# Kernel tuning notes

Hardware: AMD Instinct MI355X
Metric: run time of the kernel (lower is better)

Reference implementation:

```python
import jax, jax.numpy as jnp
import numpy as np
import math

WS = 7          # window size (hardcoded in RelativeSinusoidalEmbeddings)
NUM_HEADS = 12

def _rel_embeddings(ws=WS):
    # Faithful replica of RelativeSinusoidalEmbeddings.__init__
    C = 2 * ws - 1
    B = np.zeros((C, C), dtype=np.float32)
    positions = np.arange(C, dtype=np.float32)[:, None]
    divisor = np.exp(np.arange(0, C, 2, dtype=np.float32) * (-math.log(10000.0) / C))
    angles = positions * divisor
    B[:, 0::2] = np.sin(angles)
    B[:, 1::2] = np.cos(angles[:, :-1])
    x = np.arange(1.0, ws + 1.0, 1.0 / ws)                 # length ws*ws
    xi = (x[None, :] - x[:, None]).astype(np.int32)        # trunc toward zero, like torch .int()
    y = np.concatenate([np.arange(1, ws + 1)] * ws)
    yi = y[None, :] - y[:, None]
    return jnp.asarray(B[xi, yi])                           # [ws^2, ws^2]

def _shift_masks(ws=WS):
    n = ws * ws
    s = ws * (ws // 2)
    row = np.zeros((n, n), dtype=np.float32)
    row[-s:, : n - s] = -np.inf
    row[: n - s, -s:] = -np.inf
    # rearrange '(r w1) (c w2) -> (w1 r) (w2 c)'
    col = row.reshape(ws, ws, ws, ws).transpose(1, 0, 3, 2).reshape(n, n)
    return jnp.asarray(row), jnp.asarray(col)

_EMB = _rel_embeddings()
_ROW_MASK, _COL_MASK = _shift_masks()

def setup_inputs() -> dict:
    key = jax.random.key(0)
    k1, k2, k3 = jax.random.split(key, 3)
    B, H, W, D = 16, 56, 56, 384
    return {
        "x": jax.random.normal(k1, (B, H, W, D), dtype=jnp.float32),
        "w_qkv": jax.random.normal(k2, (D, 3 * D), dtype=jnp.float32) * 0.02,
        "b_qkv": jnp.zeros((3 * D,), dtype=jnp.float32),
        "w_out": jax.random.normal(k3, (D, D), dtype=jnp.float32) * 0.02,
        "b_out": jnp.zeros((D,), dtype=jnp.float32),
    }

def reference(x, w_qkv, b_qkv, w_out, b_out):
    B, Hh, Ww, d = x.shape
    ws, nh = WS, NUM_HEADS
    E = d // nh
    h, w = Hh // ws, Ww // ws
    # qkv projection, split last dim as (c, K=3) per rearrange 'b h w (c K)'
    qkv = (x @ w_qkv + b_qkv).reshape(B, Hh, Ww, d, 3)
    # mask is active since Hh != 7; shift is -ws//2 == -4 (faithful to source)
    qkv = jnp.roll(qkv, (-ws // 2, -ws // 2), axis=(1, 2))
    # 'b (h m1) (w m2) (H E) K -> b H h w (m1 m2) E K'
    qkv = qkv.reshape(B, h, ws, w, ws, nh, E, 3)
    qkv = qkv.transpose(0, 5, 1, 3, 2, 4, 6, 7).reshape(B, nh, h, w, ws * ws, E, 3)
    Q, K, V = qkv[..., 0], qkv[..., 1], qkv[..., 2]
    scores = jnp.einsum('bnhwqe,bnhwke->bnhwqk', Q, K) / math.sqrt(d / nh)
    scores = scores + _EMB
    scores = scores.at[:, :, -1, :].add(_ROW_MASK)   # last row of window grid
    scores = scores.at[:, :, :, -1].add(_COL_MASK)   # last col of window grid
    att = jax.nn.softmax(scores, axis=-1) @ V         # [B, nh, h, w, ws^2, E]
    # 'b H h w (m1 m2) E -> b (h m1) (w m2) (H E)'
    out = att.reshape(B, nh, h, w, ws, ws, E)
    out = out.transpose(0, 2, 4, 3, 5, 1, 6).reshape(B, Hh, Ww, d)
    out = jnp.roll(out, (ws // 2, ws // 2), axis=(1, 2))  # unshift by +3 (as in source)
    return out @ w_out + b_out
```

## Files before the change

kernel.cpp:

```cpp
#include <hip/hip_runtime.h>
#include <math.h>

#define DIM   384
#define NQKV  1152
#define IMG   56
#define ROWS_PER_B (IMG*IMG)

typedef unsigned short u16;
typedef unsigned int u32;
typedef __attribute__((ext_vector_type(4))) float f32x4;
typedef __attribute__((ext_vector_type(8))) short s16x8;

__device__ __forceinline__ u16 f2b(float f) {
    unsigned u = __float_as_uint(f);
    return (u16)((u + 0x7fffu + ((u >> 16) & 1u)) >> 16);
}

__device__ __forceinline__ void gl2lds16(const u16* g, u16* l) {
    __builtin_amdgcn_global_load_lds(
        (const __attribute__((address_space(1))) void*)g,
        (__attribute__((address_space(3))) void*)l, 16, 0, 0);
}

__global__ __launch_bounds__(256) void emb4_init_kernel(float* __restrict__ emb4) {
    int idx = blockIdx.x * 256 + threadIdx.x;
    if (idx >= 64 * 64) return;
    int q = idx >> 6, k = idx & 63;

    bool pad = (q >= 49) || (k >= 49);
    float base = 0.f;
    if (!pad) {
        const double step  = 1.0 / 7.0;
        const double delta = __dsub_rn(__dadd_rn(1.0, step), 1.0);
        double xk = __dadd_rn(1.0, __dmul_rn((double)k, delta));
        double xq = __dadd_rn(1.0, __dmul_rn((double)q, delta));
        int xi = (int)__dsub_rn(xk, xq);
        int yi = (k % 7) - (q % 7);
        int r = xi % 13; if (r < 0) r += 13;
        int c = yi % 13; if (c < 0) c += 13;
        const float scl = (float)(-0.7084877209212449);
        if ((c & 1) == 0) base = sinf((float)r * expf((float)c * scl));
        else              base = cosf((float)r * expf((float)(c - 1) * scl));
    }
    bool rmask = !pad && ((q >= 28) != (k >= 28));
    bool cmask = !pad && ((q % 7 >= 4) != (k % 7 >= 4));
    #pragma unroll
    for (int v = 0; v < 4; ++v) {
        float val = base;
        if (pad || ((v & 1) && rmask) || ((v & 2) && cmask)) val = -INFINITY;
        emb4[v * 4096 + idx] = val;
    }
}

__global__ __launch_bounds__(256) void cvt_f32_bf16(
    const float* __restrict__ in, u16* __restrict__ out, int n4) {
    int i = blockIdx.x * 256 + threadIdx.x;
    if (i >= n4) return;
    float4 v = ((const float4*)in)[i];
    ushort4 o;
    o.x = f2b(v.x); o.y = f2b(v.y); o.z = f2b(v.z); o.w = f2b(v.w);
    ((ushort4*)out)[i] = o;
}

__global__ __launch_bounds__(256) void cvt_transpose_bf16(
    const float* __restrict__ w, u16* __restrict__ wt, int R, int C) {
    int i = blockIdx.x * 256 + threadIdx.x;
    if (i >= R * C) return;
    int r = i / C, c = i % C;
    wt[(size_t)c * R + r] = f2b(w[i]);
}

__global__ __launch_bounds__(256) void cvt_transpose_qkv(
    const float* __restrict__ w, u16* __restrict__ wt) {
    int i = blockIdx.x * 256 + threadIdx.x;
    if (i >= 384 * 1152) return;
    int k = i / 1152, col = i % 1152;
    int ch = col / 3, comp = col % 3;
    int np = comp * 384 + ch;
    wt[(size_t)np * 384 + k] = f2b(w[i]);
}

__global__ __launch_bounds__(256) void bias_perm_kernel(
    const float* __restrict__ b, float* __restrict__ bp) {
    int n = blockIdx.x * 256 + threadIdx.x;
    if (n >= 1152) return;
    int comp = n / 384, ch = n % 384;
    bp[n] = b[ch * 3 + comp];
}

template <int MODE>
__global__ __launch_bounds__(256) void mfma_gemm(
    const u16* __restrict__ A, const u16* __restrict__ Bt,
    const float* __restrict__ bias,
    u16* __restrict__ outb, float* __restrict__ outf,
    int N, int K)
{
    __shared__ __align__(16) u16 As[4096];
    __shared__ __align__(16) u16 Bs[4096];

    const int tid  = threadIdx.x;
    const int lane = tid & 63;
    const int wid  = tid >> 6;
    const int wr   = wid >> 1, wc = wid & 1;
    const int l15  = lane & 15, l4 = lane >> 4;

    const int gx  = gridDim.x;
    const int nwg = gx * gridDim.y;
    int wg  = blockIdx.y * gx + blockIdx.x;
    int q8  = nwg >> 3, r8 = nwg & 7;
    int xcd = wg & 7, idx = wg >> 3;
    int nid = (xcd < r8 ? xcd * (q8 + 1) : r8 * (q8 + 1) + (xcd - r8) * q8) + idx;
    const int bm = nid / gx, bn = nid % gx;

    const int srow  = lane >> 2;
    const int sslot = (lane & 3) ^ ((srow >> 1) & 3);

    const u16* pA0 = A  + (size_t)(bm * 128 +      wid * 16 + srow) * K + sslot * 8;
    const u16* pA1 = A  + (size_t)(bm * 128 + 64 + wid * 16 + srow) * K + sslot * 8;
    const u16* pB0 = Bt + (size_t)(bn * 128 +      wid * 16 + srow) * K + sslot * 8;
    const u16* pB1 = Bt + (size_t)(bn * 128 + 64 + wid * 16 + srow) * K + sslot * 8;
    u16* lA0 = (u16*)((char*)As + wid * 1024);
    u16* lA1 = (u16*)((char*)As + 4096 + wid * 1024);
    u16* lB0 = (u16*)((char*)Bs + wid * 1024);
    u16* lB1 = (u16*)((char*)Bs + 4096 + wid * 1024);

    f32x4 acc[4][4] = {};

    for (int kt = 0; kt < K; kt += 32) {
        __syncthreads();
        gl2lds16(pA0 + kt, lA0);
        gl2lds16(pA1 + kt, lA1);
        gl2lds16(pB0 + kt, lB0);
        gl2lds16(pB1 + kt, lB1);
        __syncthreads();

        s16x8 af[4], bf[4];
        #pragma unroll
        for (int m = 0; m < 4; ++m) {
            int rm = wr * 64 + m * 16 + l15;
            af[m] = *(const s16x8*)((const char*)As + rm * 64
                                    + ((l4 ^ ((rm >> 1) & 3)) << 4));
        }
        #pragma unroll
        for (int n = 0; n < 4; ++n) {
            int rn = wc * 64 + n * 16 + l15;
            bf[n] = *(const s16x8*)((const char*)Bs + rn * 64
                                    + ((l4 ^ ((rn >> 1) & 3)) << 4));
        }
        #pragma unroll
        for (int m = 0; m < 4; ++m)
            #pragma unroll
            for (int n = 0; n < 4; ++n)
                acc[m][n] = __builtin_amdgcn_mfma_f32_16x16x32_bf16(
                    af[m], bf[n], acc[m][n], 0, 0, 0);
    }

    const int grow0 = bm * 128 + wr * 64;
    const int gcol0 = bn * 128 + wc * 64;
    #pragma unroll
    for (int m = 0; m < 4; ++m) {
        #pragma unroll
        for (int n = 0; n < 4; ++n) {
            int col = gcol0 + n * 16 + l15;
            float bz = bias[col];
            #pragma unroll
            for (int r = 0; r < 4; ++r) {
                int row = grow0 + m * 16 + l4 * 4 + r;
                float v = acc[m][n][r] + bz;
                if constexpr (MODE == 0)
                    outb[(size_t)row * N + col] = f2b(v);
                else
                    outf[(size_t)row * N + col] = v;
            }
        }
    }
}

__global__ __launch_bounds__(256) void attn_mfma_kernel(
    const u16* __restrict__ qkv, const float* __restrict__ emb4,
    u16* __restrict__ att)
{
    __shared__ __align__(16) u16 P4[4][64 * 72];
    __shared__ int rowIn[64];
    __shared__ int rowOut[64];

    const int tid  = threadIdx.x;
    const int lane = tid & 63;
    const int wid  = tid >> 6;
    const int l15  = lane & 15, l4 = lane >> 4;

    const int blk = blockIdx.x;
    const int hg  = blk % 3;
    const int win = (blk / 3) & 63;
    const int b   = blk / 192;
    const int bw  = win & 7, bh = win >> 3;
    const int head = hg * 4 + wid;

    if (tid < 64) {
        int pix = tid;
        int gr = (bh * 7 + pix / 7 + 4) % IMG;
        int gc = (bw * 7 + pix % 7 + 4) % IMG;
        rowIn[pix] = (b * IMG + gr) * IMG + gc;
    } else if (tid < 128) {
        int q = tid - 64;
        int fr = (bh * 7 + q / 7 + 3) % IMG;
        int fc = (bw * 7 + q % 7 + 3) % IMG;
        rowOut[q] = (b * IMG + fr) * IMG + fc;
    }
    __syncthreads();

    s16x8 qf[4], kf[4];
    #pragma unroll
    for (int n = 0; n < 4; ++n) {
        int pix = n * 16 + l15;
        size_t base = (size_t)rowIn[pix] * NQKV + head * 32 + l4 * 8;
        qf[n] = *(const s16x8*)(qkv + base);
        kf[n] = *(const s16x8*)(qkv + base + 384);
    }

    f32x4 sc[4][4] = {};
    #pragma unroll
    for (int m = 0; m < 4; ++m)
        #pragma unroll
        for (int n = 0; n < 4; ++n)
            sc[m][n] = __builtin_amdgcn_mfma_f32_16x16x32_bf16(
                kf[m], qf[n], sc[m][n], 0, 0, 0);

    const float scale = 0.17677669529663687f;
    const float* ev = emb4 + ((bh == 7 ? 1 : 0) + (bw == 7 ? 2 : 0)) * 4096;
    u16* P = P4[wid];
    u32* P32 = (u32*)P;

    #pragma unroll
    for (int n = 0; n < 4; ++n) {
        const int q = n * 16 + l15;
        float vals[4][4];
        float mx = -INFINITY;
        #pragma unroll
        for (int m = 0; m < 4; ++m) {
            float4 e4 = *(const float4*)(ev + q * 64 + m * 16 + l4 * 4);
            #pragma unroll
            for (int r = 0; r < 4; ++r) {
                float v = sc[m][n][r] * scale + ((const float*)&e4)[r];
                vals[m][r] = v;
                mx = fmaxf(mx, v);
            }
        }
        mx = fmaxf(mx, __shfl_xor(mx, 16));
        mx = fmaxf(mx, __shfl_xor(mx, 32));
        float sum = 0.f;
        #pragma unroll
        for (int m = 0; m < 4; ++m)
            #pragma unroll
            for (int r = 0; r < 4; ++r) {
                float p = __expf(vals[m][r] - mx);
                vals[m][r] = p;
                sum += p;
            }
        sum += __shfl_xor(sum, 16);
        sum += __shfl_xor(sum, 32);
        float inv = 1.f / sum;
        #pragma unroll
        for (int m = 0; m < 4; ++m) {
            u32 w0 = (u32)f2b(vals[m][0] * inv) | ((u32)f2b(vals[m][1] * inv) << 16);
            u32 w1 = (u32)f2b(vals[m][2] * inv) | ((u32)f2b(vals[m][3] * inv) << 16);
            int bidx = q * 36 + m * 8 + l4 * 2;
            P32[bidx]     = w0;
            P32[bidx + 1] = w1;
        }
    }

    f32x4 o[4][2] = {};
    #pragma unroll
    for (int kh = 0; kh < 2; ++kh) {
        s16x8 pf[4];
        #pragma unroll
        for (int mq = 0; mq < 4; ++mq)
            pf[mq] = *(const s16x8*)&P[(mq * 16 + l15) * 72 + kh * 32 + l4 * 8];
        s16x8 vf[2];
        #pragma unroll
        for (int ne = 0; ne < 2; ++ne) {
            #pragma unroll
            for (int j = 0; j < 8; ++j) {
                int pix = kh * 32 + l4 * 8 + j;
                vf[ne][j] = (short)qkv[(size_t)rowIn[pix] * NQKV + 768
                                       + head * 32 + ne * 16 + l15];
            }
        }
        #pragma unroll
        for (int mq = 0; mq < 4; ++mq)
            #pragma unroll
            for (int ne = 0; ne < 2; ++ne)
                o[mq][ne] = __builtin_amdgcn_mfma_f32_16x16x32_bf16(
                    pf[mq], vf[ne], o[mq][ne], 0, 0, 0);
    }

    #pragma unroll
    for (int mq = 0; mq < 4; ++mq) {
        #pragma unroll
        for (int r = 0; r < 4; ++r) {
            int q = mq * 16 + l4 * 4 + r;
            if (q < 49) {
                size_t rowb = (size_t)rowOut[q] * DIM + head * 32;
                #pragma unroll
                for (int ne = 0; ne < 2; ++ne)
                    att[rowb + ne * 16 + l15] = f2b(o[mq][ne][r]);
            }
        }
    }
}

extern "C" void kernel_launch(void* const* d_in, const int* in_sizes, int n_in,
                              void* d_out, int out_size, void* d_ws, size_t ws_size,
                              hipStream_t stream) {
    const float* x     = (const float*)d_in[0];
    const float* w_qkv = (const float*)d_in[1];
    const float* b_qkv = (const float*)d_in[2];
    const float* w_out = (const float*)d_in[3];
    const float* b_out = (const float*)d_in[4];
    float* out = (float*)d_out;

    char* wsp = (char*)d_ws;
    float* emb4  = (float*)wsp;
    u16*   wqkvt = (u16*)(wsp + 65536);
    u16*   woutt = (u16*)(wsp + 65536 + 884736);
    float* bqkvp = (float*)(wsp + 65536 + 884736 + 294912);
    const size_t fixed = 65536 + 884736 + 294912 + 4608;

    const size_t perb = (size_t)ROWS_PER_B * (DIM + NQKV + DIM) * 2;
    int nb = 16;
    while (nb > 2 && fixed + (size_t)nb * perb > ws_size) nb >>= 1;

    u16* xb   = (u16*)(wsp + fixed);
    u16* qkvb = xb   + (size_t)nb * ROWS_PER_B * DIM;
    u16* attb = qkvb + (size_t)nb * ROWS_PER_B * NQKV;

    emb4_init_kernel<<<16, 256, 0, stream>>>(emb4);
    cvt_transpose_qkv<<<(384 * 1152 + 255) / 256, 256, 0, stream>>>(w_qkv, wqkvt);
    cvt_transpose_bf16<<<(384 * 384 + 255) / 256, 256, 0, stream>>>(w_out, woutt, 384, 384);
    bias_perm_kernel<<<5, 256, 0, stream>>>(b_qkv, bqkvp);

    for (int b0 = 0; b0 < 16; b0 += nb) {
        const int rows = nb * ROWS_PER_B;
        const float* xa = x + (size_t)b0 * ROWS_PER_B * DIM;

        cvt_f32_bf16<<<(rows * DIM / 4 + 255) / 256, 256, 0, stream>>>(
            xa, xb, rows * DIM / 4);

        mfma_gemm<0><<<dim3(NQKV / 128, rows / 128), 256, 0, stream>>>(
            xb, wqkvt, bqkvp, qkvb, nullptr, NQKV, DIM);

        attn_mfma_kernel<<<nb * 192, 256, 0, stream>>>(qkvb, emb4, attb);

        mfma_gemm<1><<<dim3(DIM / 128, rows / 128), 256, 0, stream>>>(
            attb, woutt, b_out, nullptr, out + (size_t)b0 * ROWS_PER_B * DIM, DIM, DIM);
    }
}
```

Measured before the change: 184.7 us.

## Double-buffer LDS tiles in MFMA GEMM to overlap global loads with compute

Doubles the LDS A/B buffers and prefetches the next K-tile via global_load_lds while the current tile feeds the MFMAs. Explicit vmcnt waits and barriers replace the two syncthreads per iteration. This is meant to hide global memory latency in the QKV and output projection GEMMs. The cost is twice the LDS per block, which may lower occupancy, plus hand-written wait-count logic that has to be correct.

```diff
diff --git a/kernel.cpp b/kernel.cpp
--- a/kernel.cpp
+++ b/kernel.cpp
@@ -95,8 +95,8 @@
     u16* __restrict__ outb, float* __restrict__ outf,
     int N, int K)
 {
-    __shared__ __align__(16) u16 As[4096];
-    __shared__ __align__(16) u16 Bs[4096];
+    __shared__ __align__(16) u16 As[2][4096];
+    __shared__ __align__(16) u16 Bs[2][4096];
 
     const int tid  = threadIdx.x;
     const int lane = tid & 63;
@@ -119,32 +119,47 @@
     const u16* pA1 = A  + (size_t)(bm * 128 + 64 + wid * 16 + srow) * K + sslot * 8;
     const u16* pB0 = Bt + (size_t)(bn * 128 +      wid * 16 + srow) * K + sslot * 8;
     const u16* pB1 = Bt + (size_t)(bn * 128 + 64 + wid * 16 + srow) * K + sslot * 8;
-    u16* lA0 = (u16*)((char*)As + wid * 1024);
-    u16* lA1 = (u16*)((char*)As + 4096 + wid * 1024);
-    u16* lB0 = (u16*)((char*)Bs + wid * 1024);
-    u16* lB1 = (u16*)((char*)Bs + 4096 + wid * 1024);
 
     f32x4 acc[4][4] = {};
-
-    for (int kt = 0; kt < K; kt += 32) {
-        __syncthreads();
-        gl2lds16(pA0 + kt, lA0);
-        gl2lds16(pA1 + kt, lA1);
-        gl2lds16(pB0 + kt, lB0);
-        gl2lds16(pB1 + kt, lB1);
-        __syncthreads();
+    const int NT = K >> 5;
+
+    {
+        u16* a0 = (u16*)((char*)As[0] + wid * 1024);
+        u16* a1 = (u16*)((char*)As[0] + 4096 + wid * 1024);
+        u16* b0 = (u16*)((char*)Bs[0] + wid * 1024);
+        u16* b1 = (u16*)((char*)Bs[0] + 4096 + wid * 1024);
+        gl2lds16(pA0, a0); gl2lds16(pA1, a1);
+        gl2lds16(pB0, b0); gl2lds16(pB1, b1);
+    }
+
+    for (int t = 0; t < NT; ++t) {
+        const int buf = t & 1;
+        if (t + 1 < NT) {
+            const int kt1 = (t + 1) << 5;
+            u16* a0 = (u16*)((char*)As[buf ^ 1] + wid * 1024);
+            u16* a1 = (u16*)((char*)As[buf ^ 1] + 4096 + wid * 1024);
+            u16* b0 = (u16*)((char*)Bs[buf ^ 1] + wid * 1024);
+            u16* b1 = (u16*)((char*)Bs[buf ^ 1] + 4096 + wid * 1024);
+            gl2lds16(pA0 + kt1, a0); gl2lds16(pA1 + kt1, a1);
+            gl2lds16(pB0 + kt1, b0); gl2lds16(pB1 + kt1, b1);
+            asm volatile("s_waitcnt vmcnt(4)" ::: "memory");
+        } else {
+            asm volatile("s_waitcnt vmcnt(0)" ::: "memory");
+        }
+        __builtin_amdgcn_s_barrier();
+        __builtin_amdgcn_sched_barrier(0);
 
         s16x8 af[4], bf[4];
         #pragma unroll
         for (int m = 0; m < 4; ++m) {
             int rm = wr * 64 + m * 16 + l15;
-            af[m] = *(const s16x8*)((const char*)As + rm * 64
+            af[m] = *(const s16x8*)((const char*)As[buf] + rm * 64
                                     + ((l4 ^ ((rm >> 1) & 3)) << 4));
         }
         #pragma unroll
         for (int n = 0; n < 4; ++n) {
             int rn = wc * 64 + n * 16 + l15;
-            bf[n] = *(const s16x8*)((const char*)Bs + rn * 64
+            bf[n] = *(const s16x8*)((const char*)Bs[buf] + rn * 64
                                     + ((l4 ^ ((rn >> 1) & 3)) << 4));
         }
         #pragma unroll
@@ -153,6 +168,10 @@
             for (int n = 0; n < 4; ++n)
                 acc[m][n] = __builtin_amdgcn_mfma_f32_16x16x32_bf16(
                     af[m], bf[n], acc[m][n], 0, 0, 0);
+
+        asm volatile("s_waitcnt lgkmcnt(0)" ::: "memory");
+        __builtin_amdgcn_sched_barrier(0);
+        __builtin_amdgcn_s_barrier();
     }
 
     const int grow0 = bm * 128 + wr * 64;
```

Measured after the change: 182.0 us. Within noise of the previous version (-1.4%).
